# Performance work log

Measured on AMD Instinct MI355X. Metric: run time of the kernel, lower is better.

Reference implementation:

```python
import jax, jax.numpy as jnp
import numpy as np

B, L, K1, P = 16, 224, 8192, 16  # batch, spectral bands, pixels, endmembers
LEAKY_SLOPE = 0.01  # torch nn.LeakyReLU default


def setup_inputs() -> dict:
    key = jax.random.key(0)
    ks = jax.random.split(key, 7)
    return {
        "a": jax.random.normal(ks[0], (B, P, K1), jnp.float32),
        "d2": jax.random.normal(ks[1], (B, P, K1), jnp.float32),
        "y": jax.random.normal(ks[2], (B, L, K1), jnp.float32),
        "w3_w": jax.random.normal(ks[3], (P, P), jnp.float32) * 0.1,  # Conv1d(P,P,1) weight squeezed
        "b3_w": jax.random.normal(ks[4], (P, P), jnp.float32) * 0.1,
        "w3_c": jax.random.normal(ks[5], (1, L, P), jnp.float32),     # kernel codebook
        "sigma": jnp.ones((1,), jnp.float32) * 2.0,
        "ca_w": jax.random.normal(ks[6], (2, P), jnp.float32) * 0.1,  # CA Conv1d(P,2,1) weight squeezed
    }


def reference(a, d2, y, w3_w, b3_w, w3_c, sigma, ca_w):
    # h2 = Conv1d(P,P,1)(a - d2)  -> pointwise matmul over channel dim
    h2 = jnp.einsum('pq,bqn->bpn', w3_w, a - d2)  # (B,P,K1)

    # GaussianKernelLayer: pairwise L2 distances between y pixels (B,L,K1)
    # and codebook columns w3_c (1,L,P), via the GEMM identity
    # ||u-v||^2 = ||u||^2 + ||v||^2 - 2 u.v  (avoids the (B,L,K1,P) broadcast).
    y_sq = jnp.sum(y * y, axis=1)            # (B,K1)
    c_sq = jnp.sum(w3_c * w3_c, axis=1)      # (1,P)
    cross = jnp.einsum('blk,olp->bkp', y, w3_c)  # (B,K1,P)
    dist_sq = jnp.maximum(y_sq[:, :, None] + c_sq[:, None, :] - 2.0 * cross, 0.0)
    dist = jnp.sqrt(dist_sq)                 # (B,K1,P)
    h3 = jnp.exp(-0.5 * jnp.square(dist / sigma[0]))
    h3 = jnp.transpose(h3, (0, 2, 1))        # (B,P,K1)

    # CA channel attention: avg/max pool over pixels -> Conv1d(P,2,1) -> LeakyReLU -> softmax
    avg = jnp.mean(h3, axis=-1)              # (B,P)
    mx = jnp.max(h3, axis=-1)                # (B,P)
    conv_lrelu = lambda v: jax.nn.leaky_relu(jnp.einsum('cp,bp->bc', ca_w, v), LEAKY_SLOPE)
    ratio = jax.nn.softmax(conv_lrelu(avg) + conv_lrelu(mx), axis=-1)  # (B,2)

    # combine center pixel + mean pixel via bmm with ratio
    mid = h3[:, :, K1 // 2]                  # (B,P)
    mean = jnp.mean(h3, axis=-1)             # (B,P)
    stacked = jnp.stack([mid, mean], axis=1)  # (B,2,P)
    comb = jnp.einsum('bc,bcp->bp', ratio, stacked)  # (B,P)

    # h4 = Conv1d(P,P,1)(comb[:, :, None])
    h4 = jnp.einsum('pq,bq->bp', b3_w, comb)[:, :, None]  # (B,P,1)

    return h4 + h2  # broadcast over pixel dim -> (B,P,K1)
```

## Files before the change

kernel.cpp:

```cpp
#include <hip/hip_runtime.h>

#define Bn  16
#define Ln  224
#define K1n 8192
#define Pn  16
#define NCHUNK 32


__device__ __forceinline__ float readlane_f(float v, int lane) {
    return __uint_as_float(__builtin_amdgcn_readlane(__float_as_uint(v), lane));
}

__global__ __launch_bounds__(256) void k_stats(
    const float* __restrict__ y,
    const float* __restrict__ w3c,
    const float* __restrict__ sigma,
    float* __restrict__ ws_sum,
    float* __restrict__ ws_max,
    float* __restrict__ ws_mid)
{
    __shared__ float s_csq_part[16][Pn];
    __shared__ float s_csq[Pn];
    __shared__ float s_part_s[4][Pn];
    __shared__ float s_part_m[4][Pn];

    const int tid   = threadIdx.x;
    const int lane  = tid & 63;
    const int b     = blockIdx.x >> 5;
    const int chunk = blockIdx.x & 31;
    const int k     = (chunk << 8) + tid;

    {
        const int p   = tid & 15;
        const int sub = tid >> 4;
        float cs = 0.f;
#pragma unroll
        for (int l = sub; l < Ln; l += 16) {
            float v = w3c[l * Pn + p];
            cs = fmaf(v, v, cs);
        }
        s_csq_part[sub][p] = cs;
    }
    __syncthreads();
    if (tid < Pn) {
        float cs = 0.f;
#pragma unroll
        for (int s = 0; s < 16; ++s) cs += s_csq_part[s][tid];
        s_csq[tid] = cs;
    }
    __syncthreads();

    float cross[Pn];
#pragma unroll
    for (int p = 0; p < Pn; ++p) cross[p] = 0.f;
    float ysq = 0.f;

    const float* yp = y + (size_t)b * Ln * K1n + k;

    float wv = w3c[lane];
#pragma unroll 2
    for (int q = 0; q < Ln / 4; ++q) {
        float wv_next = (q < Ln / 4 - 1) ? w3c[(q + 1) * 64 + lane] : 0.f;
        float v0 = yp[(size_t)(4 * q + 0) * K1n];
        float v1 = yp[(size_t)(4 * q + 1) * K1n];
        float v2 = yp[(size_t)(4 * q + 2) * K1n];
        float v3 = yp[(size_t)(4 * q + 3) * K1n];

        ysq = fmaf(v0, v0, ysq);
        ysq = fmaf(v1, v1, ysq);
        ysq = fmaf(v2, v2, ysq);
        ysq = fmaf(v3, v3, ysq);

#pragma unroll
        for (int p = 0; p < Pn; ++p) {
            cross[p] = fmaf(v0, readlane_f(wv,  0 * 16 + p), cross[p]);
            cross[p] = fmaf(v1, readlane_f(wv,  1 * 16 + p), cross[p]);
            cross[p] = fmaf(v2, readlane_f(wv,  2 * 16 + p), cross[p]);
            cross[p] = fmaf(v3, readlane_f(wv,  3 * 16 + p), cross[p]);
        }
        wv = wv_next;
    }

    const float sg = sigma[0];
    const float nh = -0.5f / (sg * sg);

    float h3[Pn];
#pragma unroll
    for (int p = 0; p < Pn; ++p) {
        float d = fmaxf(ysq + s_csq[p] - 2.f * cross[p], 0.f);
        h3[p] = __expf(d * nh);
    }

    if (k == (K1n / 2)) {
#pragma unroll
        for (int p = 0; p < Pn; ++p) ws_mid[b * Pn + p] = h3[p];
    }

    const int wv_id = tid >> 6;
#pragma unroll
    for (int p = 0; p < Pn; ++p) {
        float s = h3[p];
        float m = h3[p];
#pragma unroll
        for (int off = 32; off > 0; off >>= 1) {
            s += __shfl_down(s, off, 64);
            m = fmaxf(m, __shfl_down(m, off, 64));
        }
        if (lane == 0) { s_part_s[wv_id][p] = s; s_part_m[wv_id][p] = m; }
    }
    __syncthreads();
    if (tid < Pn) {
        float s = s_part_s[0][tid] + s_part_s[1][tid] + s_part_s[2][tid] + s_part_s[3][tid];
        float m = fmaxf(fmaxf(s_part_m[0][tid], s_part_m[1][tid]),
                        fmaxf(s_part_m[2][tid], s_part_m[3][tid]));
        const int base = (b * NCHUNK + chunk) * Pn + tid;
        ws_sum[base] = s;
        ws_max[base] = m;
    }
}

__global__ __launch_bounds__(256) void k_out(
    const float* __restrict__ a,
    const float* __restrict__ d2,
    const float* __restrict__ w3w,
    const float* __restrict__ b3w,
    const float* __restrict__ caw,
    const float* __restrict__ ws_sum,
    const float* __restrict__ ws_max,
    const float* __restrict__ ws_mid,
    float* __restrict__ out)
{
    __shared__ float s_w3w[Pn][Pn];
    __shared__ float s_red_s[16][Pn];
    __shared__ float s_red_m[16][Pn];
    __shared__ float s_avg[Pn], s_mx[Pn], s_mid[Pn], s_comb[Pn], s_h4[Pn];
    __shared__ float s_t[2];

    const int tid = threadIdx.x;
    const int b   = blockIdx.x >> 5;
    const int k   = ((blockIdx.x & 31) << 8) + tid;

    if (tid < Pn * Pn) s_w3w[tid >> 4][tid & 15] = w3w[tid];

    {
        const int p   = tid & 15;
        const int grp = tid >> 4;
        const int i0  = (b * NCHUNK + grp)      * Pn + p;
        const int i1  = (b * NCHUNK + grp + 16) * Pn + p;
        s_red_s[grp][p] = ws_sum[i0] + ws_sum[i1];
        s_red_m[grp][p] = fmaxf(ws_max[i0], ws_max[i1]);
    }
    __syncthreads();
    if (tid < Pn) {
        float s = 0.f, m = -1.f;
        for (int g = 0; g < 16; ++g) {
            s += s_red_s[g][tid];
            m = fmaxf(m, s_red_m[g][tid]);
        }
        s_avg[tid] = s * (1.f / (float)K1n);
        s_mx[tid]  = m;
        s_mid[tid] = ws_mid[b * Pn + tid];
    }
    __syncthreads();

    if (tid < 2) {
        float t1 = 0.f, t2 = 0.f;
        for (int p = 0; p < Pn; ++p) {
            float cw = caw[tid * Pn + p];
            t1 = fmaf(cw, s_avg[p], t1);
            t2 = fmaf(cw, s_mx[p],  t2);
        }
        t1 = (t1 > 0.f) ? t1 : 0.01f * t1;
        t2 = (t2 > 0.f) ? t2 : 0.01f * t2;
        s_t[tid] = t1 + t2;
    }
    __syncthreads();

    if (tid < Pn) {
        float t0 = s_t[0], u1 = s_t[1];
        float mt = fmaxf(t0, u1);
        float e0 = __expf(t0 - mt), e1 = __expf(u1 - mt);
        float inv = 1.f / (e0 + e1);
        s_comb[tid] = (e0 * inv) * s_mid[tid] + (e1 * inv) * s_avg[tid];
    }
    __syncthreads();

    if (tid < Pn) {
        float h = 0.f;
        for (int q = 0; q < Pn; ++q) h = fmaf(b3w[tid * Pn + q], s_comb[q], h);
        s_h4[tid] = h;
    }
    __syncthreads();

    const size_t base = (size_t)b * Pn * K1n + (size_t)k;
    float diff[Pn];
#pragma unroll
    for (int q = 0; q < Pn; ++q) {
        float av = a [base + (size_t)q * K1n];
        float dv = d2[base + (size_t)q * K1n];
        diff[q] = av - dv;
    }
#pragma unroll
    for (int p = 0; p < Pn; ++p) {
        float h2 = 0.f;
#pragma unroll
        for (int q = 0; q < Pn; ++q) h2 = fmaf(s_w3w[p][q], diff[q], h2);
        out[base + (size_t)p * K1n] = h2 + s_h4[p];
    }
}

extern "C" void kernel_launch(void* const* d_in, const int* in_sizes, int n_in,
                              void* d_out, int out_size, void* d_ws, size_t ws_size,
                              hipStream_t stream) {
    const float* a     = (const float*)d_in[0];
    const float* d2    = (const float*)d_in[1];
    const float* y     = (const float*)d_in[2];
    const float* w3w   = (const float*)d_in[3];
    const float* b3w   = (const float*)d_in[4];
    const float* w3c   = (const float*)d_in[5];
    const float* sigma = (const float*)d_in[6];
    const float* caw   = (const float*)d_in[7];

    float* ws_sum = (float*)d_ws;
    float* ws_max = ws_sum + Bn * NCHUNK * Pn;
    float* ws_mid = ws_max + Bn * NCHUNK * Pn;

    k_stats<<<dim3(Bn * NCHUNK), dim3(256), 0, stream>>>(
        y, w3c, sigma, ws_sum, ws_max, ws_mid);

    k_out<<<dim3(Bn * NCHUNK), dim3(256), 0, stream>>>(
        a, d2, w3w, b3w, caw, ws_sum, ws_max, ws_mid, (float*)d_out);
}
```

Baseline: 218.8 us.

## Double-buffer y tiles into LDS with async global_load_lds in stats kernel

The stats kernel now streams y in chunks of 28 bands into a double-buffered LDS tile using direct global-to-LDS async loads, prefetching the next chunk while computing the current one. Codebook weights are also prefetched per chunk in registers. The goal is to hide global memory latency on the dominant y read. In exchange it adds LDS usage (about 57KB), which lowers occupancy, plus a barrier per chunk. It also relies on the barrier to order the async LDS writes without an explicit wait on outstanding loads, and one earlier barrier was removed, which raises correctness risk.

```diff
diff --git a/kernel.cpp b/kernel.cpp
--- a/kernel.cpp
+++ b/kernel.cpp
@@ -5,10 +5,17 @@
 #define K1n 8192
 #define Pn  16
 #define NCHUNK 32
+#define CH  28
 
 
 __device__ __forceinline__ float readlane_f(float v, int lane) {
     return __uint_as_float(__builtin_amdgcn_readlane(__float_as_uint(v), lane));
+}
+
+__device__ __forceinline__ void async_copy_dword(const float* g, float* l) {
+    __builtin_amdgcn_global_load_lds(
+        (const __attribute__((address_space(1))) unsigned int*)g,
+        (__attribute__((address_space(3))) unsigned int*)l, 4, 0, 0);
 }
 
 __global__ __launch_bounds__(256) void k_stats(
@@ -19,6 +26,7 @@
     float* __restrict__ ws_max,
     float* __restrict__ ws_mid)
 {
+    __shared__ float s_y[2][CH][256];
     __shared__ float s_csq_part[16][Pn];
     __shared__ float s_csq[Pn];
     __shared__ float s_part_s[4][Pn];
@@ -26,6 +34,7 @@
 
     const int tid   = threadIdx.x;
     const int lane  = tid & 63;
+    const int wv    = tid >> 6;
     const int b     = blockIdx.x >> 5;
     const int chunk = blockIdx.x & 31;
     const int k     = (chunk << 8) + tid;
@@ -48,37 +57,54 @@
         for (int s = 0; s < 16; ++s) cs += s_csq_part[s][tid];
         s_csq[tid] = cs;
     }
-    __syncthreads();
 
     float cross[Pn];
 #pragma unroll
     for (int p = 0; p < Pn; ++p) cross[p] = 0.f;
     float ysq = 0.f;
 
-    const float* yp = y + (size_t)b * Ln * K1n + k;
-
-    float wv = w3c[lane];
-#pragma unroll 2
-    for (int q = 0; q < Ln / 4; ++q) {
-        float wv_next = (q < Ln / 4 - 1) ? w3c[(q + 1) * 64 + lane] : 0.f;
-        float v0 = yp[(size_t)(4 * q + 0) * K1n];
-        float v1 = yp[(size_t)(4 * q + 1) * K1n];
-        float v2 = yp[(size_t)(4 * q + 2) * K1n];
-        float v3 = yp[(size_t)(4 * q + 3) * K1n];
-
-        ysq = fmaf(v0, v0, ysq);
-        ysq = fmaf(v1, v1, ysq);
-        ysq = fmaf(v2, v2, ysq);
-        ysq = fmaf(v3, v3, ysq);
-
-#pragma unroll
-        for (int p = 0; p < Pn; ++p) {
-            cross[p] = fmaf(v0, readlane_f(wv,  0 * 16 + p), cross[p]);
-            cross[p] = fmaf(v1, readlane_f(wv,  1 * 16 + p), cross[p]);
-            cross[p] = fmaf(v2, readlane_f(wv,  2 * 16 + p), cross[p]);
-            cross[p] = fmaf(v3, readlane_f(wv,  3 * 16 + p), cross[p]);
-        }
-        wv = wv_next;
+    const float* ybase = y + (size_t)b * Ln * K1n + (chunk << 8) + (wv << 6) + lane;
+
+    float wq[7], wqn[7];
+#pragma unroll
+    for (int q = 0; q < 7; ++q) wq[q] = w3c[q * 64 + lane];
+
+    for (int l = 0; l < CH; ++l)
+        async_copy_dword(ybase + (size_t)l * K1n, &s_y[0][l][wv << 6]);
+    __syncthreads();
+
+    for (int c = 0; c < Ln / CH; ++c) {
+        const int cb = c & 1;
+        if (c < Ln / CH - 1) {
+            const int nb = cb ^ 1;
+#pragma unroll
+            for (int q = 0; q < 7; ++q)
+                wqn[q] = w3c[((c + 1) * CH) * Pn + q * 64 + lane];
+            for (int l = 0; l < CH; ++l)
+                async_copy_dword(ybase + (size_t)((c + 1) * CH + l) * K1n,
+                                 &s_y[nb][l][wv << 6]);
+        }
+#pragma unroll
+        for (int q = 0; q < 7; ++q) {
+            float v0 = s_y[cb][q * 4 + 0][tid];
+            float v1 = s_y[cb][q * 4 + 1][tid];
+            float v2 = s_y[cb][q * 4 + 2][tid];
+            float v3 = s_y[cb][q * 4 + 3][tid];
+            ysq = fmaf(v0, v0, ysq);
+            ysq = fmaf(v1, v1, ysq);
+            ysq = fmaf(v2, v2, ysq);
+            ysq = fmaf(v3, v3, ysq);
+#pragma unroll
+            for (int p = 0; p < Pn; ++p) {
+                cross[p] = fmaf(v0, readlane_f(wq[q],  0 + p), cross[p]);
+                cross[p] = fmaf(v1, readlane_f(wq[q], 16 + p), cross[p]);
+                cross[p] = fmaf(v2, readlane_f(wq[q], 32 + p), cross[p]);
+                cross[p] = fmaf(v3, readlane_f(wq[q], 48 + p), cross[p]);
+            }
+        }
+#pragma unroll
+        for (int q = 0; q < 7; ++q) wq[q] = wqn[q];
+        __syncthreads();
     }
 
     const float sg = sigma[0];
@@ -96,7 +122,6 @@
         for (int p = 0; p < Pn; ++p) ws_mid[b * Pn + p] = h3[p];
     }
 
-    const int wv_id = tid >> 6;
 #pragma unroll
     for (int p = 0; p < Pn; ++p) {
         float s = h3[p];
@@ -106,7 +131,7 @@
             s += __shfl_down(s, off, 64);
             m = fmaxf(m, __shfl_down(m, off, 64));
         }
-        if (lane == 0) { s_part_s[wv_id][p] = s; s_part_m[wv_id][p] = m; }
+        if (lane == 0) { s_part_s[wv][p] = s; s_part_m[wv][p] = m; }
     }
     __syncthreads();
     if (tid < Pn) {
```

Result: faster. 214.1 us (-2.1%).
